# Kernel tuning notes

Measured on AMD Instinct MI355X. Metric: run time of the kernel, lower is better.

## Reference

```python
import jax, jax.numpy as jnp
import numpy as np

B, T, D, H = 4, 2048, 1024, 16
HD = D // H  # head_dim = 64

def setup_inputs() -> dict:
    key = jax.random.key(0)
    k1, k2, k3 = jax.random.split(key, 3)
    s = 1.0 / np.sqrt(D)
    return {
        "x": jax.random.normal(k1, (B, T, D), dtype=jnp.float32),
        "w_qkv": jax.random.normal(k2, (D, 3 * D), dtype=jnp.float32) * s,
        "b_qkv": jnp.zeros((3 * D,), dtype=jnp.float32),
        "w_proj": jax.random.normal(k3, (D, D), dtype=jnp.float32) * s,
        "b_proj": jnp.zeros((D,), dtype=jnp.float32),
    }

def reference(x, w_qkv, b_qkv, w_proj, b_proj):
    b, t, c = x.shape
    qkv = x @ w_qkv + b_qkv                       # [B,T,3D]
    qkv = qkv.reshape(b, t, 3, H, HD)
    q, k, v = (jnp.transpose(qkv[:, :, i], (0, 2, 1, 3)) for i in range(3))  # [B,H,T,HD]
    scale = 1.0 / np.sqrt(HD)
    attn = jnp.einsum('bhqd,bhkd->bhqk', q, k) * scale  # [B,H,T,T]
    attn = jax.nn.softmax(attn, axis=-1)
    out = jnp.einsum('bhqk,bhkd->bhqd', attn, v)        # [B,H,T,HD]
    out = jnp.transpose(out, (0, 2, 1, 3)).reshape(b, t, c)
    return out @ w_proj + b_proj
```

## Files before the change

### kernel.cpp

```cpp
#include <hip/hip_runtime.h>
#include <hip/hip_bf16.h>

#define T_SEQ   2048
#define D_MODEL 1024
#define N_HEADS 16
#define HEAD_DIM 64
#define BT      8192
#define N3D     3072

using short8  = __attribute__((ext_vector_type(8))) short;
using short4v = __attribute__((ext_vector_type(4))) short;
using floatx4 = __attribute__((ext_vector_type(4))) float;

#define QSCALE 0.18033688f

__device__ __forceinline__ unsigned short rne_bf16(float f) {
  unsigned int u = __float_as_uint(f);
  u = (u + 0x7fffu + ((u >> 16) & 1u)) >> 16;
  return (unsigned short)u;
}
__device__ __forceinline__ float bf_to_f(unsigned short s) {
  return __uint_as_float(((unsigned int)s) << 16);
}

__device__ __forceinline__ void gload_lds16(const unsigned short* g,
                                            unsigned short* l) {
  __builtin_amdgcn_global_load_lds(
      (const __attribute__((address_space(1))) void*)g,
      (__attribute__((address_space(3))) void*)l, 16, 0, 0);
}

__global__ __launch_bounds__(256) void k_convert(const float* __restrict__ in,
                                                 unsigned short* __restrict__ out) {
  size_t i = ((size_t)blockIdx.x * 256 + threadIdx.x) * 8;
  float4 a = *(const float4*)(in + i);
  float4 b = *(const float4*)(in + i + 4);
  short8 v;
  v[0] = (short)rne_bf16(a.x); v[1] = (short)rne_bf16(a.y);
  v[2] = (short)rne_bf16(a.z); v[3] = (short)rne_bf16(a.w);
  v[4] = (short)rne_bf16(b.x); v[5] = (short)rne_bf16(b.y);
  v[6] = (short)rne_bf16(b.z); v[7] = (short)rne_bf16(b.w);
  *(short8*)(((short*)out) + i) = v;
}

__global__ __launch_bounds__(256) void k_transpose_convert(
    const float* __restrict__ in, unsigned short* __restrict__ out_hi,
    int R, int C) {
  __shared__ float tile[64][65];
  int tiles_c = C >> 6;
  int r0 = (blockIdx.x / tiles_c) << 6;
  int c0 = (blockIdx.x % tiles_c) << 6;
  int tid = threadIdx.x;
#pragma unroll
  for (int i = 0; i < 16; ++i) {
    int idx = tid + i * 256;
    int r = idx >> 6, c = idx & 63;
    tile[r][c] = in[(size_t)(r0 + r) * C + c0 + c];
  }
  __syncthreads();
#pragma unroll
  for (int i = 0; i < 16; ++i) {
    int idx = tid + i * 256;
    int orow = idx >> 6, oc = idx & 63;
    out_hi[(size_t)(c0 + orow) * R + r0 + oc] = rne_bf16(tile[oc][orow]);
  }
}

__global__ __launch_bounds__(256) void k_qkv_gemm(
    const unsigned short* __restrict__ A, const unsigned short* __restrict__ Bt,
    const float* __restrict__ bias,
    unsigned short* __restrict__ Qo, unsigned short* __restrict__ Ko,
    unsigned short* __restrict__ Vt) {
  __shared__ __align__(16) unsigned short As[128 * 32];
  __shared__ __align__(16) unsigned short Bs[128 * 32];
  int tid = threadIdx.x;
  int m0 = (blockIdx.x / 24) * 128;
  int n0 = (blockIdx.x % 24) * 128;
  int w = tid >> 6, lane = tid & 63, quad = lane >> 4, l16 = lane & 15;
  int wm = (w >> 1) * 64, wn = (w & 1) * 64;
  floatx4 acc[4][4] = {};

  int s_row[2], s_sp[2];
#pragma unroll
  for (int i = 0; i < 2; ++i) {
    int u = tid + i * 256;
    s_row[i] = u >> 2;
    s_sp[i] = (u & 3) ^ ((s_row[i] >> 1) & 3);
  }
  int a_off[4], b_off[4];
#pragma unroll
  for (int t = 0; t < 4; ++t) {
    int ra = wm + t * 16 + l16, rb = wn + t * 16 + l16;
    a_off[t] = ra * 32 + (quad ^ ((ra >> 1) & 3)) * 8;
    b_off[t] = rb * 32 + (quad ^ ((rb >> 1) & 3)) * 8;
  }

  for (int k0 = 0; k0 < 1024; k0 += 32) {
#pragma unroll
    for (int i = 0; i < 2; ++i) {
      int ub = (tid & ~63) + i * 256;
      gload_lds16(A + (size_t)(m0 + s_row[i]) * 1024 + k0 + s_sp[i] * 8,
                  &As[ub * 8]);
      gload_lds16(Bt + (size_t)(n0 + s_row[i]) * 1024 + k0 + s_sp[i] * 8,
                  &Bs[ub * 8]);
    }
    __syncthreads();
    short8 af[4], bf[4];
#pragma unroll
    for (int mt = 0; mt < 4; ++mt) af[mt] = *(const short8*)(&As[a_off[mt]]);
#pragma unroll
    for (int nt = 0; nt < 4; ++nt) bf[nt] = *(const short8*)(&Bs[b_off[nt]]);
#pragma unroll
    for (int mt = 0; mt < 4; ++mt)
#pragma unroll
      for (int nt = 0; nt < 4; ++nt)
        acc[mt][nt] = __builtin_amdgcn_mfma_f32_16x16x32_bf16(af[mt], bf[nt],
                                                              acc[mt][nt], 0, 0, 0);
    __syncthreads();
  }

#pragma unroll
  for (int nt = 0; nt < 4; ++nt) {
    int n = n0 + wn + nt * 16 + l16;
    float bv = bias[n];
    int which = n >> 10;
    int nn = n & 1023;
    int h = nn >> 6, hd = nn & 63;
#pragma unroll
    for (int mt = 0; mt < 4; ++mt) {
      int mbase = m0 + wm + mt * 16 + quad * 4;
      int b = mbase >> 11;
      int t0 = mbase & 2047;
      int head = b * N_HEADS + h;
      if (which == 2) {
        short4v vv;
#pragma unroll
        for (int r = 0; r < 4; ++r) vv[r] = (short)rne_bf16(acc[mt][nt][r] + bv);
        *(short4v*)(&Vt[((size_t)head * HEAD_DIM + hd) * T_SEQ + t0]) = vv;
      } else {
        unsigned short* dst = (which == 0) ? Qo : Ko;
        float scl = (which == 0) ? QSCALE : 1.0f;
#pragma unroll
        for (int r = 0; r < 4; ++r)
          dst[((size_t)head * T_SEQ + t0 + r) * HEAD_DIM + hd] =
              rne_bf16((acc[mt][nt][r] + bv) * scl);
      }
    }
  }
}

__global__ __launch_bounds__(256) void k_attn(
    const unsigned short* __restrict__ Q, const unsigned short* __restrict__ K,
    const unsigned short* __restrict__ Vt, unsigned short* __restrict__ Oo) {
  __shared__ __align__(16) unsigned short Klds[64 * 64];
  __shared__ __align__(16) unsigned short Vlds[64 * 64];
  __shared__ __align__(16) unsigned short Plds[4][16 * 64];
  int tid = threadIdx.x;
  int head = blockIdx.x >> 5;
  int qb = (blockIdx.x & 31) << 6;
  int b = head >> 4, h = head & 15;
  int w = tid >> 6, lane = tid & 63, quad = lane >> 4, l16 = lane & 15;
  const unsigned short* Qh = Q + (size_t)head * T_SEQ * HEAD_DIM;
  const unsigned short* Kh = K + (size_t)head * T_SEQ * HEAD_DIM;
  const unsigned short* Vh = Vt + (size_t)head * HEAD_DIM * T_SEQ;

  int qrow = qb + w * 16 + l16;
  short8 qf[2];
  qf[0] = *(const short8*)(Qh + (size_t)qrow * 64 + quad * 8);
  qf[1] = *(const short8*)(Qh + (size_t)qrow * 64 + 32 + quad * 8);

  short8 ones;
#pragma unroll
  for (int j = 0; j < 8; ++j) ones[j] = (short)0x3F80;

  floatx4 O[4] = {};
  floatx4 Osum = {};

  int sg[2], sidx[2], sub[2];
#pragma unroll
  for (int i = 0; i < 2; ++i) {
    sg[i] = (tid + i * 256) >> 6;
    sidx[i] = lane ^ sg[i];
    sub[i] = (tid & ~63) + i * 256;
  }

  for (int kb = 0; kb < 32; ++kb) {
#pragma unroll
    for (int i = 0; i < 2; ++i) {
      gload_lds16(Kh + ((size_t)(kb * 64 + sidx[i])) * 64 + sg[i] * 8,
                  &Klds[sub[i] * 8]);
      gload_lds16(Vh + (size_t)sidx[i] * T_SEQ + kb * 64 + sg[i] * 8,
                  &Vlds[sub[i] * 8]);
    }
    __syncthreads();

    floatx4 s[4] = {};
#pragma unroll
    for (int ks = 0; ks < 2; ++ks) {
      int gk = ks * 4 + quad;
#pragma unroll
      for (int nt = 0; nt < 4; ++nt) {
        int PU = ((gk << 6) + nt * 16 + l16) ^ gk;
        short8 kf = *(const short8*)(&Klds[PU * 8]);
        s[nt] = __builtin_amdgcn_mfma_f32_16x16x32_bf16(qf[ks], kf, s[nt], 0, 0, 0);
      }
    }

#pragma unroll
    for (int nt = 0; nt < 4; ++nt) {
      int key = nt * 16 + l16;
      int kg = key >> 3;
      int e = key & 7;
      int U0 = kg * 16 + quad * 4;
      float p0 = __builtin_amdgcn_exp2f(s[nt][0]);
      float p1 = __builtin_amdgcn_exp2f(s[nt][1]);
      float p2 = __builtin_amdgcn_exp2f(s[nt][2]);
      float p3 = __builtin_amdgcn_exp2f(s[nt][3]);
      __hip_bfloat162 lo2 = __float22bfloat162_rn(make_float2(p0, p1));
      __hip_bfloat162 hi2 = __float22bfloat162_rn(make_float2(p2, p3));
      unsigned int blo = *(unsigned int*)&lo2;
      unsigned int bhi = *(unsigned int*)&hi2;
      Plds[w][((U0 + 0) ^ kg) * 8 + e] = (unsigned short)blo;
      Plds[w][((U0 + 1) ^ kg) * 8 + e] = (unsigned short)(blo >> 16);
      Plds[w][((U0 + 2) ^ kg) * 8 + e] = (unsigned short)bhi;
      Plds[w][((U0 + 3) ^ kg) * 8 + e] = (unsigned short)(bhi >> 16);
    }

#pragma unroll
    for (int ks = 0; ks < 2; ++ks) {
      int gk = ks * 4 + quad;
      int PUp = ((gk << 4) + l16) ^ gk;
      short8 pf = *(const short8*)(&Plds[w][PUp * 8]);
      Osum = __builtin_amdgcn_mfma_f32_16x16x32_bf16(pf, ones, Osum, 0, 0, 0);
#pragma unroll
      for (int dt = 0; dt < 4; ++dt) {
        int PUv = ((gk << 6) + dt * 16 + l16) ^ gk;
        short8 vf = *(const short8*)(&Vlds[PUv * 8]);
        O[dt] = __builtin_amdgcn_mfma_f32_16x16x32_bf16(pf, vf, O[dt], 0, 0, 0);
      }
    }
    __syncthreads();
  }

  float inv[4];
#pragma unroll
  for (int r = 0; r < 4; ++r) inv[r] = 1.0f / Osum[r];
#pragma unroll
  for (int dt = 0; dt < 4; ++dt)
#pragma unroll
    for (int r = 0; r < 4; ++r) {
      float val = O[dt][r] * inv[r];
      int t = qb + w * 16 + quad * 4 + r;
      size_t o = ((size_t)(b * T_SEQ + t)) * D_MODEL + h * HEAD_DIM + dt * 16 + l16;
      Oo[o] = rne_bf16(val);
    }
}

__global__ __launch_bounds__(256) void k_proj_gemm(
    const unsigned short* __restrict__ A, const unsigned short* __restrict__ Bt,
    const float* __restrict__ bias, float* __restrict__ out) {
  __shared__ __align__(16) unsigned short As[128 * 32];
  __shared__ __align__(16) unsigned short Bs[128 * 32];
  int tid = threadIdx.x;
  int m0 = (blockIdx.x >> 3) * 128;
  int n0 = (blockIdx.x & 7) * 128;
  int w = tid >> 6, lane = tid & 63, quad = lane >> 4, l16 = lane & 15;
  int wm = (w >> 1) * 64, wn = (w & 1) * 64;
  floatx4 acc[4][4] = {};

  int s_row[2], s_sp[2];
#pragma unroll
  for (int i = 0; i < 2; ++i) {
    int u = tid + i * 256;
    s_row[i] = u >> 2;
    s_sp[i] = (u & 3) ^ ((s_row[i] >> 1) & 3);
  }
  int a_off[4], b_off[4];
#pragma unroll
  for (int t = 0; t < 4; ++t) {
    int ra = wm + t * 16 + l16, rb = wn + t * 16 + l16;
    a_off[t] = ra * 32 + (quad ^ ((ra >> 1) & 3)) * 8;
    b_off[t] = rb * 32 + (quad ^ ((rb >> 1) & 3)) * 8;
  }

  for (int k0 = 0; k0 < 1024; k0 += 32) {
#pragma unroll
    for (int i = 0; i < 2; ++i) {
      int ub = (tid & ~63) + i * 256;
      gload_lds16(A + (size_t)(m0 + s_row[i]) * 1024 + k0 + s_sp[i] * 8,
                  &As[ub * 8]);
      gload_lds16(Bt + (size_t)(n0 + s_row[i]) * 1024 + k0 + s_sp[i] * 8,
                  &Bs[ub * 8]);
    }
    __syncthreads();
    short8 af[4], bf[4];
#pragma unroll
    for (int mt = 0; mt < 4; ++mt) af[mt] = *(const short8*)(&As[a_off[mt]]);
#pragma unroll
    for (int nt = 0; nt < 4; ++nt) bf[nt] = *(const short8*)(&Bs[b_off[nt]]);
#pragma unroll
    for (int mt = 0; mt < 4; ++mt)
#pragma unroll
      for (int nt = 0; nt < 4; ++nt)
        acc[mt][nt] = __builtin_amdgcn_mfma_f32_16x16x32_bf16(af[mt], bf[nt],
                                                              acc[mt][nt], 0, 0, 0);
    __syncthreads();
  }

#pragma unroll
  for (int nt = 0; nt < 4; ++nt) {
    int n = n0 + wn + nt * 16 + l16;
    float bv = bias[n];
#pragma unroll
    for (int mt = 0; mt < 4; ++mt)
#pragma unroll
      for (int r = 0; r < 4; ++r) {
        int m = m0 + wm + mt * 16 + quad * 4 + r;
        out[(size_t)m * 1024 + n] = acc[mt][nt][r] + bv;
      }
  }
}

extern "C" void kernel_launch(void* const* d_in, const int* in_sizes, int n_in,
                              void* d_out, int out_size, void* d_ws, size_t ws_size,
                              hipStream_t stream) {
  const float* x     = (const float*)d_in[0];
  const float* wqkv  = (const float*)d_in[1];
  const float* bqkv  = (const float*)d_in[2];
  const float* wproj = (const float*)d_in[3];
  const float* bproj = (const float*)d_in[4];

  char* ws = (char*)d_ws;
  size_t off = 0;
  unsigned short* x_bf  = (unsigned short*)(ws + off); off += (size_t)BT * D_MODEL * 2;
  unsigned short* wq_T  = (unsigned short*)(ws + off); off += (size_t)N3D * D_MODEL * 2;
  unsigned short* wp_T  = (unsigned short*)(ws + off); off += (size_t)D_MODEL * D_MODEL * 2;
  unsigned short* Qb    = (unsigned short*)(ws + off); off += (size_t)BT * D_MODEL * 2;
  unsigned short* Kb    = (unsigned short*)(ws + off); off += (size_t)BT * D_MODEL * 2;
  unsigned short* Vt    = (unsigned short*)(ws + off); off += (size_t)BT * D_MODEL * 2;
  unsigned short* a_bf  = (unsigned short*)(ws + off); off += (size_t)BT * D_MODEL * 2;

  k_convert<<<(BT * D_MODEL) / (256 * 8), 256, 0, stream>>>(x, x_bf);
  k_transpose_convert<<<(1024 / 64) * (3072 / 64), 256, 0, stream>>>(wqkv, wq_T, 1024, 3072);
  k_transpose_convert<<<(1024 / 64) * (1024 / 64), 256, 0, stream>>>(wproj, wp_T, 1024, 1024);
  k_qkv_gemm<<<(BT / 128) * (N3D / 128), 256, 0, stream>>>(x_bf, wq_T, bqkv, Qb, Kb, Vt);
  k_attn<<<(T_SEQ / 64) * 4 * N_HEADS, 256, 0, stream>>>(Qb, Kb, Vt, a_bf);
  k_proj_gemm<<<(BT / 128) * (D_MODEL / 128), 256, 0, stream>>>(a_bf, wp_T, bproj, (float*)d_out);
}
```

Baseline: 332.8 us.

## Process 128 query rows per attention block to reuse K/V tiles

Each wave now handles two 16-row query sub-tiles instead of one, so an attention block covers 128 queries and the grid halves. Every K/V tile staged in LDS is reused across twice as many queries, which halves global K/V traffic and the number of barriers per query. The trade-offs are more registers per thread (two sets of S/O accumulators), a larger P scratch buffer in LDS, and fewer blocks, which may lower occupancy.

```diff
diff --git a/kernel.cpp b/kernel.cpp
--- a/kernel.cpp
+++ b/kernel.cpp
@@ -18,9 +18,6 @@
   unsigned int u = __float_as_uint(f);
   u = (u + 0x7fffu + ((u >> 16) & 1u)) >> 16;
   return (unsigned short)u;
-}
-__device__ __forceinline__ float bf_to_f(unsigned short s) {
-  return __uint_as_float(((unsigned int)s) << 16);
 }
 
 __device__ __forceinline__ void gload_lds16(const unsigned short* g,
@@ -154,27 +151,32 @@
     const unsigned short* __restrict__ Vt, unsigned short* __restrict__ Oo) {
   __shared__ __align__(16) unsigned short Klds[64 * 64];
   __shared__ __align__(16) unsigned short Vlds[64 * 64];
-  __shared__ __align__(16) unsigned short Plds[4][16 * 64];
+  __shared__ __align__(16) unsigned short Plds[4][2][16 * 64];
   int tid = threadIdx.x;
-  int head = blockIdx.x >> 5;
-  int qb = (blockIdx.x & 31) << 6;
+  int head = blockIdx.x >> 4;
+  int qb = (blockIdx.x & 15) << 7;
   int b = head >> 4, h = head & 15;
   int w = tid >> 6, lane = tid & 63, quad = lane >> 4, l16 = lane & 15;
   const unsigned short* Qh = Q + (size_t)head * T_SEQ * HEAD_DIM;
   const unsigned short* Kh = K + (size_t)head * T_SEQ * HEAD_DIM;
   const unsigned short* Vh = Vt + (size_t)head * HEAD_DIM * T_SEQ;
 
-  int qrow = qb + w * 16 + l16;
-  short8 qf[2];
-  qf[0] = *(const short8*)(Qh + (size_t)qrow * 64 + quad * 8);
-  qf[1] = *(const short8*)(Qh + (size_t)qrow * 64 + 32 + quad * 8);
+  short8 qf[2][2];
+#pragma unroll
+  for (int qi = 0; qi < 2; ++qi) {
+    int qrow = qb + w * 32 + qi * 16 + l16;
+#pragma unroll
+    for (int ks = 0; ks < 2; ++ks)
+      qf[qi][ks] = *(const short8*)(Qh + (size_t)qrow * 64 + ks * 32 + quad * 8);
+  }
 
   short8 ones;
 #pragma unroll
   for (int j = 0; j < 8; ++j) ones[j] = (short)0x3F80;
 
-  floatx4 O[4] = {};
-  floatx4 Osum = {};
+  floatx4 O[2][4] = {};
+  floatx4 Osum[2] = {};
+  const floatx4 zf = {};
 
   int sg[2], sidx[2], sub[2];
 #pragma unroll
@@ -194,7 +196,7 @@
     }
     __syncthreads();
 
-    floatx4 s[4] = {};
+    floatx4 s[2][4];
 #pragma unroll
     for (int ks = 0; ks < 2; ++ks) {
       int gk = ks * 4 + quad;
@@ -202,58 +204,73 @@
       for (int nt = 0; nt < 4; ++nt) {
         int PU = ((gk << 6) + nt * 16 + l16) ^ gk;
         short8 kf = *(const short8*)(&Klds[PU * 8]);
-        s[nt] = __builtin_amdgcn_mfma_f32_16x16x32_bf16(qf[ks], kf, s[nt], 0, 0, 0);
-      }
-    }
-
-#pragma unroll
-    for (int nt = 0; nt < 4; ++nt) {
-      int key = nt * 16 + l16;
-      int kg = key >> 3;
-      int e = key & 7;
-      int U0 = kg * 16 + quad * 4;
-      float p0 = __builtin_amdgcn_exp2f(s[nt][0]);
-      float p1 = __builtin_amdgcn_exp2f(s[nt][1]);
-      float p2 = __builtin_amdgcn_exp2f(s[nt][2]);
-      float p3 = __builtin_amdgcn_exp2f(s[nt][3]);
-      __hip_bfloat162 lo2 = __float22bfloat162_rn(make_float2(p0, p1));
-      __hip_bfloat162 hi2 = __float22bfloat162_rn(make_float2(p2, p3));
-      unsigned int blo = *(unsigned int*)&lo2;
-      unsigned int bhi = *(unsigned int*)&hi2;
-      Plds[w][((U0 + 0) ^ kg) * 8 + e] = (unsigned short)blo;
-      Plds[w][((U0 + 1) ^ kg) * 8 + e] = (unsigned short)(blo >> 16);
-      Plds[w][((U0 + 2) ^ kg) * 8 + e] = (unsigned short)bhi;
-      Plds[w][((U0 + 3) ^ kg) * 8 + e] = (unsigned short)(bhi >> 16);
+        if (ks == 0) {
+          s[0][nt] = __builtin_amdgcn_mfma_f32_16x16x32_bf16(qf[0][0], kf, zf, 0, 0, 0);
+          s[1][nt] = __builtin_amdgcn_mfma_f32_16x16x32_bf16(qf[1][0], kf, zf, 0, 0, 0);
+        } else {
+          s[0][nt] = __builtin_amdgcn_mfma_f32_16x16x32_bf16(qf[0][1], kf, s[0][nt], 0, 0, 0);
+          s[1][nt] = __builtin_amdgcn_mfma_f32_16x16x32_bf16(qf[1][1], kf, s[1][nt], 0, 0, 0);
+        }
+      }
+    }
+
+#pragma unroll
+    for (int qi = 0; qi < 2; ++qi) {
+#pragma unroll
+      for (int nt = 0; nt < 4; ++nt) {
+        int key = nt * 16 + l16;
+        int kg = key >> 3;
+        int e = key & 7;
+        int U0 = kg * 16 + quad * 4;
+        float p0 = __builtin_amdgcn_exp2f(s[qi][nt][0]);
+        float p1 = __builtin_amdgcn_exp2f(s[qi][nt][1]);
+        float p2 = __builtin_amdgcn_exp2f(s[qi][nt][2]);
+        float p3 = __builtin_amdgcn_exp2f(s[qi][nt][3]);
+        __hip_bfloat162 lo2 = __float22bfloat162_rn(make_float2(p0, p1));
+        __hip_bfloat162 hi2 = __float22bfloat162_rn(make_float2(p2, p3));
+        unsigned int blo = *(unsigned int*)&lo2;
+        unsigned int bhi = *(unsigned int*)&hi2;
+        Plds[w][qi][((U0 + 0) ^ kg) * 8 + e] = (unsigned short)blo;
+        Plds[w][qi][((U0 + 1) ^ kg) * 8 + e] = (unsigned short)(blo >> 16);
+        Plds[w][qi][((U0 + 2) ^ kg) * 8 + e] = (unsigned short)bhi;
+        Plds[w][qi][((U0 + 3) ^ kg) * 8 + e] = (unsigned short)(bhi >> 16);
+      }
     }
 
 #pragma unroll
     for (int ks = 0; ks < 2; ++ks) {
       int gk = ks * 4 + quad;
       int PUp = ((gk << 4) + l16) ^ gk;
-      short8 pf = *(const short8*)(&Plds[w][PUp * 8]);
-      Osum = __builtin_amdgcn_mfma_f32_16x16x32_bf16(pf, ones, Osum, 0, 0, 0);
+      short8 pf0 = *(const short8*)(&Plds[w][0][PUp * 8]);
+      short8 pf1 = *(const short8*)(&Plds[w][1][PUp * 8]);
+      Osum[0] = __builtin_amdgcn_mfma_f32_16x16x32_bf16(pf0, ones, Osum[0], 0, 0, 0);
+      Osum[1] = __builtin_amdgcn_mfma_f32_16x16x32_bf16(pf1, ones, Osum[1], 0, 0, 0);
 #pragma unroll
       for (int dt = 0; dt < 4; ++dt) {
         int PUv = ((gk << 6) + dt * 16 + l16) ^ gk;
         short8 vf = *(const short8*)(&Vlds[PUv * 8]);
-        O[dt] = __builtin_amdgcn_mfma_f32_16x16x32_bf16(pf, vf, O[dt], 0, 0, 0);
-      }
-    }
-    __syncthreads();
-  }
-
-  float inv[4];
-#pragma unroll
-  for (int r = 0; r < 4; ++r) inv[r] = 1.0f / Osum[r];
-#pragma unroll
-  for (int dt = 0; dt < 4; ++dt)
-#pragma unroll
-    for (int r = 0; r < 4; ++r) {
-      float val = O[dt][r] * inv[r];
-      int t = qb + w * 16 + quad * 4 + r;
-      size_t o = ((size_t)(b * T_SEQ + t)) * D_MODEL + h * HEAD_DIM + dt * 16 + l16;
-      Oo[o] = rne_bf16(val);
-    }
+        O[0][dt] = __builtin_amdgcn_mfma_f32_16x16x32_bf16(pf0, vf, O[0][dt], 0, 0, 0);
+        O[1][dt] = __builtin_amdgcn_mfma_f32_16x16x32_bf16(pf1, vf, O[1][dt], 0, 0, 0);
+      }
+    }
+    __syncthreads();
+  }
+
+#pragma unroll
+  for (int qi = 0; qi < 2; ++qi) {
+    float inv[4];
+#pragma unroll
+    for (int r = 0; r < 4; ++r) inv[r] = 1.0f / Osum[qi][r];
+#pragma unroll
+    for (int dt = 0; dt < 4; ++dt)
+#pragma unroll
+      for (int r = 0; r < 4; ++r) {
+        float val = O[qi][dt][r] * inv[r];
+        int t = qb + w * 32 + qi * 16 + quad * 4 + r;
+        size_t o = ((size_t)(b * T_SEQ + t)) * D_MODEL + h * HEAD_DIM + dt * 16 + l16;
+        Oo[o] = rne_bf16(val);
+      }
+  }
 }
 
 __global__ __launch_bounds__(256) void k_proj_gemm(
@@ -344,6 +361,6 @@
   k_transpose_convert<<<(1024 / 64) * (3072 / 64), 256, 0, stream>>>(wqkv, wq_T, 1024, 3072);
   k_transpose_convert<<<(1024 / 64) * (1024 / 64), 256, 0, stream>>>(wproj, wp_T, 1024, 1024);
   k_qkv_gemm<<<(BT / 128) * (N3D / 128), 256, 0, stream>>>(x_bf, wq_T, bqkv, Qb, Kb, Vt);
-  k_attn<<<(T_SEQ / 64) * 4 * N_HEADS, 256, 0, stream>>>(Qb, Kb, Vt, a_bf);
+  k_attn<<<(T_SEQ / 128) * 4 * N_HEADS, 256, 0, stream>>>(Qb, Kb, Vt, a_bf);
   k_proj_gemm<<<(BT / 128) * (D_MODEL / 128), 256, 0, stream>>>(a_bf, wp_T, bproj, (float*)d_out);
 }
```

Result: no change. 333.8 us (+0.3%).
